# Performance work log

Measured on AMD Instinct MI355X. Metric: run time of the kernel, lower is better.

Reference implementation:

```python
import jax, jax.numpy as jnp
import numpy as np

B_, N, C = 4096, 49, 128
H = 4          # num_heads
NW = 64        # windows per image


def setup_inputs() -> dict:
    key = jax.random.key(0)
    k = jax.random.split(key, 6)
    s = 0.02
    return {
        "x": jax.random.normal(k[0], (B_, N, C), jnp.float32),
        "mask": jax.random.normal(k[1], (NW, N, N), jnp.float32),
        "qkv_w": jax.random.normal(k[2], (3 * C, C), jnp.float32) * s,
        "qkv_b": jax.random.normal(k[3], (3 * C,), jnp.float32) * s,
        "proj_w": jax.random.normal(k[4], (C, C), jnp.float32) * s,
        "proj_b": jax.random.normal(k[5], (C,), jnp.float32) * s,
    }


def reference(x, mask, qkv_w, qkv_b, proj_w, proj_b):
    b, n, c = x.shape
    hd = c // H
    scale = hd ** -0.5
    # fused QKV projection: [b, n, 3, H, hd] -> [3, b, H, n, hd]
    qkv = (x @ qkv_w.T + qkv_b).reshape(b, n, 3, H, hd)
    qkv = jnp.transpose(qkv, (2, 0, 3, 1, 4))
    q, k, v = qkv[0] * scale, qkv[1], qkv[2]
    attn = jnp.einsum("bhnd,bhmd->bhnm", q, k)  # [b, H, n, n]
    nW = mask.shape[0]
    attn = attn.reshape(b // nW, nW, H, n, n) + mask[None, :, None, :, :]
    attn = jax.nn.softmax(attn.reshape(b, H, n, n), axis=-1)
    out = jnp.einsum("bhnm,bhmd->bhnd", attn, v)
    out = jnp.transpose(out, (0, 2, 1, 3)).reshape(b, n, c)
    return out @ proj_w.T + proj_b
```

## Files before the change

kernel.cpp:

```cpp
#include <hip/hip_runtime.h>
#include <hip/hip_bf16.h>

#define C_DIM 128
#define SCALE 0.17677669529663687f

typedef __attribute__((ext_vector_type(8))) short frag8;
typedef __attribute__((ext_vector_type(4))) float f32x4;

#define HEAD_SZ 7424
#define Q_STR 40
#define VT_STR 72
#define P_STR 72
#define XBF_STR 136
#define SMEM_TOT 29696

__device__ __forceinline__ unsigned short f2b(float x) {
    __hip_bfloat16 h = __float2bfloat16(x);
    return __builtin_bit_cast(unsigned short, h);
}
__device__ __forceinline__ unsigned pk2(float a, float b) {
    return ((unsigned)f2b(b) << 16) | (unsigned)f2b(a);
}

__global__ void convert_weights(const float4* __restrict__ qkvw,
                                const float4* __restrict__ projw,
                                ushort4* __restrict__ wbf) {
    int i = blockIdx.x * 256 + threadIdx.x;
    float4 v = (i < 12288) ? qkvw[i] : projw[i - 12288];
    ushort4 p;
    p.x = f2b(v.x); p.y = f2b(v.y); p.z = f2b(v.z); p.w = f2b(v.w);
    wbf[i] = p;
}

__global__ __launch_bounds__(512, 4) void attn_mfma(
    const float* __restrict__ x,
    const float* __restrict__ mask,
    const float* __restrict__ qkv_b,
    const float* __restrict__ proj_b,
    const unsigned short* __restrict__ wq,
    float* __restrict__ out)
{
    __shared__ __align__(16) unsigned short sm[SMEM_TOT];

    const int b = blockIdx.x, tid = threadIdx.x;
    const int wave = tid >> 6;
    const int h    = wave >> 1;
    const int half = wave & 1;
    const int lane = tid & 63;
    const int n16  = lane & 15;
    const int q    = lane >> 4;

    {
        const float4* xg = (const float4*)(x + (size_t)b * 6272);
        for (int i = tid; i < 1568; i += 512) {
            float4 v = xg[i];
            int row = i >> 5, col = (i & 31) << 2;
            uint2 pk; pk.x = pk2(v.x, v.y); pk.y = pk2(v.z, v.w);
            *(uint2*)&sm[row * XBF_STR + col] = pk;
        }
        if (tid < 510) *(ushort4*)&sm[49 * XBF_STR + tid * 4] = (ushort4){0, 0, 0, 0};
    }
    __syncthreads();

    frag8 xf[2][4];
#pragma unroll
    for (int tt = 0; tt < 2; ++tt)
#pragma unroll
        for (int ks = 0; ks < 4; ++ks)
            xf[tt][ks] = *(const frag8*)&sm[((half * 2 + tt) * 16 + n16) * XBF_STR + ks * 32 + q * 8];
    __syncthreads();

    const int Qb = h * HEAD_SZ, Kb = Qb + 2560, Vb = Qb + 5120, Pb = Qb;

#pragma unroll
    for (int mat = 0; mat < 3; ++mat) {
#pragma unroll
        for (int ct = 0; ct < 2; ++ct) {
            const unsigned short* wrow = wq + (size_t)(mat * C_DIM + h * 32 + ct * 16 + n16) * C_DIM;
            frag8 wf[4];
#pragma unroll
            for (int ks = 0; ks < 4; ++ks) wf[ks] = *(const frag8*)(wrow + ks * 32 + q * 8);
            if (mat < 2) {
                float4 b4 = *(const float4*)(qkv_b + mat * C_DIM + h * 32 + ct * 16 + q * 4);
                const float sc = (mat == 0) ? SCALE : 1.f;
                const int base = (mat == 0) ? Qb : Kb;
#pragma unroll
                for (int tt = 0; tt < 2; ++tt) {
                    f32x4 acc = {0.f, 0.f, 0.f, 0.f};
#pragma unroll
                    for (int ks = 0; ks < 4; ++ks)
                        acc = __builtin_amdgcn_mfma_f32_16x16x32_bf16(wf[ks], xf[tt][ks], acc, 0, 0, 0);
                    uint2 pk;
                    pk.x = pk2((acc[0] + b4.x) * sc, (acc[1] + b4.y) * sc);
                    pk.y = pk2((acc[2] + b4.z) * sc, (acc[3] + b4.w) * sc);
                    *(uint2*)&sm[base + ((half * 2 + tt) * 16 + n16) * Q_STR + ct * 16 + q * 4] = pk;
                }
            } else {
                float bias = qkv_b[2 * C_DIM + h * 32 + ct * 16 + n16];
#pragma unroll
                for (int tt = 0; tt < 2; ++tt) {
                    f32x4 acc = {0.f, 0.f, 0.f, 0.f};
#pragma unroll
                    for (int ks = 0; ks < 4; ++ks)
                        acc = __builtin_amdgcn_mfma_f32_16x16x32_bf16(xf[tt][ks], wf[ks], acc, 0, 0, 0);
                    uint2 pk;
                    pk.x = pk2(acc[0] + bias, acc[1] + bias);
                    pk.y = pk2(acc[2] + bias, acc[3] + bias);
                    *(uint2*)&sm[Vb + (ct * 16 + n16) * VT_STR + (half * 2 + tt) * 16 + q * 4] = pk;
                }
            }
        }
    }
    __syncthreads();

    frag8 qf[2], kf[4];
#pragma unroll
    for (int it = 0; it < 2; ++it)
        qf[it] = *(const frag8*)&sm[Qb + ((half * 2 + it) * 16 + n16) * Q_STR + q * 8];
#pragma unroll
    for (int jt = 0; jt < 4; ++jt)
        kf[jt] = *(const frag8*)&sm[Kb + (jt * 16 + n16) * Q_STR + q * 8];
    __syncthreads();

    const float* mrow = mask + (size_t)(b & 63) * 2401;
    int ii[2];
#pragma unroll
    for (int it = 0; it < 2; ++it) ii[it] = min(half * 32 + it * 16 + n16, 48);

    f32x4 s[4][2];
#pragma unroll
    for (int it = 0; it < 2; ++it) {
#pragma unroll
        for (int jt = 0; jt < 3; ++jt) {
            const float* mp = mrow + ii[it] * 49 + jt * 16 + q * 4;
            s[jt][it] = (f32x4){mp[0], mp[1], mp[2], mp[3]};
        }
        float m48 = (q == 0) ? mrow[ii[it] * 49 + 48] : 0.f;
        s[3][it] = (f32x4){m48, 0.f, 0.f, 0.f};
    }
#pragma unroll
    for (int jt = 0; jt < 4; ++jt)
#pragma unroll
        for (int it = 0; it < 2; ++it)
            s[jt][it] = __builtin_amdgcn_mfma_f32_16x16x32_bf16(kf[jt], qf[it], s[jt][it], 0, 0, 0);

#pragma unroll
    for (int it = 0; it < 2; ++it) {
        float mx = -1e30f;
#pragma unroll
        for (int jt = 0; jt < 4; ++jt)
#pragma unroll
            for (int r = 0; r < 4; ++r)
                if (jt * 16 + q * 4 + r < 49) mx = fmaxf(mx, s[jt][it][r]);
        mx = fmaxf(mx, __shfl_xor(mx, 16));
        mx = fmaxf(mx, __shfl_xor(mx, 32));
        float sum = 0.f;
#pragma unroll
        for (int jt = 0; jt < 4; ++jt)
#pragma unroll
            for (int r = 0; r < 4; ++r) {
                float e = (jt * 16 + q * 4 + r < 49) ? __expf(s[jt][it][r] - mx) : 0.f;
                s[jt][it][r] = e;
                sum += e;
            }
        sum += __shfl_xor(sum, 16);
        sum += __shfl_xor(sum, 32);
        float inv = __builtin_amdgcn_rcpf(sum);
#pragma unroll
        for (int jt = 0; jt < 4; ++jt) {
            uint2 pk;
            pk.x = pk2(s[jt][it][0] * inv, s[jt][it][1] * inv);
            pk.y = pk2(s[jt][it][2] * inv, s[jt][it][3] * inv);
            *(uint2*)&sm[Pb + (half * 32 + it * 16 + n16) * P_STR + jt * 16 + q * 4] = pk;
        }
    }

    frag8 vf[2][2];
#pragma unroll
    for (int ct = 0; ct < 2; ++ct)
#pragma unroll
        for (int ks = 0; ks < 2; ++ks)
            vf[ct][ks] = *(const frag8*)&sm[Vb + (ct * 16 + n16) * VT_STR + ks * 32 + q * 8];
    f32x4 o[2][2];
#pragma unroll
    for (int ct = 0; ct < 2; ++ct)
#pragma unroll
        for (int nt = 0; nt < 2; ++nt) o[ct][nt] = (f32x4){0.f, 0.f, 0.f, 0.f};
#pragma unroll
    for (int nt = 0; nt < 2; ++nt)
#pragma unroll
        for (int ks = 0; ks < 2; ++ks) {
            frag8 pf = *(const frag8*)&sm[Pb + ((half * 2 + nt) * 16 + n16) * P_STR + ks * 32 + q * 8];
#pragma unroll
            for (int ct = 0; ct < 2; ++ct)
                o[ct][nt] = __builtin_amdgcn_mfma_f32_16x16x32_bf16(vf[ct][ks], pf, o[ct][nt], 0, 0, 0);
        }
    __syncthreads();

#pragma unroll
    for (int ct = 0; ct < 2; ++ct)
#pragma unroll
        for (int nt = 0; nt < 2; ++nt) {
            uint2 pk;
            pk.x = pk2(o[ct][nt][0], o[ct][nt][1]);
            pk.y = pk2(o[ct][nt][2], o[ct][nt][3]);
            *(uint2*)&sm[((half * 2 + nt) * 16 + n16) * XBF_STR + h * 32 + ct * 16 + q * 4] = pk;
        }
    __syncthreads();

    const unsigned short* pw = wq + 49152;
    frag8 wf2[4];
#pragma unroll
    for (int ks = 0; ks < 4; ++ks)
        wf2[ks] = *(const frag8*)(pw + (size_t)(wave * 16 + n16) * C_DIM + ks * 32 + q * 8);
    float4 b4 = *(const float4*)(proj_b + wave * 16 + q * 4);
    float* outb = out + (size_t)b * 6272;
#pragma unroll
    for (int nt = 0; nt < 4; ++nt) {
        f32x4 acc = {0.f, 0.f, 0.f, 0.f};
#pragma unroll
        for (int ks = 0; ks < 4; ++ks) {
            frag8 af = *(const frag8*)&sm[(nt * 16 + n16) * XBF_STR + ks * 32 + q * 8];
            acc = __builtin_amdgcn_mfma_f32_16x16x32_bf16(wf2[ks], af, acc, 0, 0, 0);
        }
        int tok = nt * 16 + n16;
        if (tok < 49)
            *(float4*)&outb[tok * C_DIM + wave * 16 + q * 4] =
                make_float4(acc[0] + b4.x, acc[1] + b4.y, acc[2] + b4.z, acc[3] + b4.w);
    }
}

extern "C" void kernel_launch(void* const* d_in, const int* in_sizes, int n_in,
                              void* d_out, int out_size, void* d_ws, size_t ws_size,
                              hipStream_t stream) {
    const float* x      = (const float*)d_in[0];
    const float* mask   = (const float*)d_in[1];
    const float* qkv_b  = (const float*)d_in[3];
    const float* proj_b = (const float*)d_in[5];

    unsigned short* wbf = (unsigned short*)d_ws;
    convert_weights<<<64, 256, 0, stream>>>((const float4*)d_in[2],
                                            (const float4*)d_in[4],
                                            (ushort4*)wbf);
    attn_mfma<<<4096, 512, 0, stream>>>(x, mask, qkv_b, proj_b, wbf, (float*)d_out);
}
```

Baseline: 293.1 us.

## Use one wave per head with 256-thread blocks and fewer barriers

Changes the block from 8 waves (two per head, each handling half the tokens) to 4 waves, one per head, so each wave computes all 49 tokens for its head. This removes several block-wide barriers, because Q/K/V/P stay private to each wave, and the per-head buffers now live beyond the activation buffer so x no longer has to be rewritten. The projection weights and biases are loaded at kernel start to hide global latency, and each wave computes two output column tiles. In exchange, each wave holds more registers (xf[4][4], s[4][4], wf2) and there are fewer waves per block, which may reduce latency hiding and occupancy.

```diff
diff --git a/kernel.cpp b/kernel.cpp
--- a/kernel.cpp
+++ b/kernel.cpp
@@ -7,12 +7,15 @@
 typedef __attribute__((ext_vector_type(8))) short frag8;
 typedef __attribute__((ext_vector_type(4))) float f32x4;
 
-#define HEAD_SZ 7424
+#define XACT_STR 136
+#define HEAD_OFF 6800
+#define HEAD_SZ  6304
+#define KOFF 2000
+#define VOFF 4000
 #define Q_STR 40
 #define VT_STR 72
 #define P_STR 72
-#define XBF_STR 136
-#define SMEM_TOT 29696
+#define SMEM_TOT 32016
 
 __device__ __forceinline__ unsigned short f2b(float x) {
     __hip_bfloat16 h = __float2bfloat16(x);
@@ -32,7 +35,7 @@
     wbf[i] = p;
 }
 
-__global__ __launch_bounds__(512, 4) void attn_mfma(
+__global__ __launch_bounds__(256, 2) void attn_mfma(
     const float* __restrict__ x,
     const float* __restrict__ mask,
     const float* __restrict__ qkv_b,
@@ -43,34 +46,43 @@
     __shared__ __align__(16) unsigned short sm[SMEM_TOT];
 
     const int b = blockIdx.x, tid = threadIdx.x;
-    const int wave = tid >> 6;
-    const int h    = wave >> 1;
-    const int half = wave & 1;
+    const int h    = tid >> 6;
     const int lane = tid & 63;
     const int n16  = lane & 15;
     const int q    = lane >> 4;
 
+    const unsigned short* pw = wq + 49152;
+    frag8 wf2[2][4];
+#pragma unroll
+    for (int ct = 0; ct < 2; ++ct)
+#pragma unroll
+        for (int ks = 0; ks < 4; ++ks)
+            wf2[ct][ks] = *(const frag8*)(pw + (size_t)(h * 32 + ct * 16 + n16) * C_DIM + ks * 32 + q * 8);
+    float4 pb4[2];
+#pragma unroll
+    for (int ct = 0; ct < 2; ++ct)
+        pb4[ct] = *(const float4*)(proj_b + h * 32 + ct * 16 + q * 4);
+
     {
         const float4* xg = (const float4*)(x + (size_t)b * 6272);
-        for (int i = tid; i < 1568; i += 512) {
+        for (int i = tid; i < 1568; i += 256) {
             float4 v = xg[i];
             int row = i >> 5, col = (i & 31) << 2;
             uint2 pk; pk.x = pk2(v.x, v.y); pk.y = pk2(v.z, v.w);
-            *(uint2*)&sm[row * XBF_STR + col] = pk;
-        }
-        if (tid < 510) *(ushort4*)&sm[49 * XBF_STR + tid * 4] = (ushort4){0, 0, 0, 0};
+            *(uint2*)&sm[row * XACT_STR + col] = pk;
+        }
     }
     __syncthreads();
 
-    frag8 xf[2][4];
-#pragma unroll
-    for (int tt = 0; tt < 2; ++tt)
+    frag8 xf[4][4];
+#pragma unroll
+    for (int tt = 0; tt < 4; ++tt)
 #pragma unroll
         for (int ks = 0; ks < 4; ++ks)
-            xf[tt][ks] = *(const frag8*)&sm[((half * 2 + tt) * 16 + n16) * XBF_STR + ks * 32 + q * 8];
+            xf[tt][ks] = *(const frag8*)&sm[min(tt * 16 + n16, 48) * XACT_STR + ks * 32 + q * 8];
     __syncthreads();
 
-    const int Qb = h * HEAD_SZ, Kb = Qb + 2560, Vb = Qb + 5120, Pb = Qb;
+    const int Hb = HEAD_OFF + h * HEAD_SZ;
 
 #pragma unroll
     for (int mat = 0; mat < 3; ++mat) {
@@ -83,9 +95,9 @@
             if (mat < 2) {
                 float4 b4 = *(const float4*)(qkv_b + mat * C_DIM + h * 32 + ct * 16 + q * 4);
                 const float sc = (mat == 0) ? SCALE : 1.f;
-                const int base = (mat == 0) ? Qb : Kb;
-#pragma unroll
-                for (int tt = 0; tt < 2; ++tt) {
+                const int base = Hb + ((mat == 0) ? 0 : KOFF);
+#pragma unroll
+                for (int tt = 0; tt < 4; ++tt) {
                     f32x4 acc = {0.f, 0.f, 0.f, 0.f};
 #pragma unroll
                     for (int ks = 0; ks < 4; ++ks)
@@ -93,12 +105,12 @@
                     uint2 pk;
                     pk.x = pk2((acc[0] + b4.x) * sc, (acc[1] + b4.y) * sc);
                     pk.y = pk2((acc[2] + b4.z) * sc, (acc[3] + b4.w) * sc);
-                    *(uint2*)&sm[base + ((half * 2 + tt) * 16 + n16) * Q_STR + ct * 16 + q * 4] = pk;
+                    *(uint2*)&sm[base + min(tt * 16 + n16, 49) * Q_STR + ct * 16 + q * 4] = pk;
                 }
             } else {
                 float bias = qkv_b[2 * C_DIM + h * 32 + ct * 16 + n16];
 #pragma unroll
-                for (int tt = 0; tt < 2; ++tt) {
+                for (int tt = 0; tt < 4; ++tt) {
                     f32x4 acc = {0.f, 0.f, 0.f, 0.f};
 #pragma unroll
                     for (int ks = 0; ks < 4; ++ks)
@@ -106,46 +118,39 @@
                     uint2 pk;
                     pk.x = pk2(acc[0] + bias, acc[1] + bias);
                     pk.y = pk2(acc[2] + bias, acc[3] + bias);
-                    *(uint2*)&sm[Vb + (ct * 16 + n16) * VT_STR + (half * 2 + tt) * 16 + q * 4] = pk;
+                    *(uint2*)&sm[Hb + VOFF + (ct * 16 + n16) * VT_STR + tt * 16 + q * 4] = pk;
                 }
             }
         }
     }
-    __syncthreads();
-
-    frag8 qf[2], kf[4];
-#pragma unroll
-    for (int it = 0; it < 2; ++it)
-        qf[it] = *(const frag8*)&sm[Qb + ((half * 2 + it) * 16 + n16) * Q_STR + q * 8];
+
+    frag8 qf[4], kf[4];
+#pragma unroll
+    for (int t = 0; t < 4; ++t) {
+        qf[t] = *(const frag8*)&sm[Hb + (t * 16 + n16) * Q_STR + q * 8];
+        kf[t] = *(const frag8*)&sm[Hb + KOFF + (t * 16 + n16) * Q_STR + q * 8];
+    }
+    const float* mrow = mask + (size_t)(b & 63) * 2401;
+    f32x4 s[4][4];
+#pragma unroll
+    for (int it = 0; it < 4; ++it) {
+        int ii = min(it * 16 + n16, 48);
+#pragma unroll
+        for (int jt = 0; jt < 3; ++jt) {
+            const float* mp = mrow + ii * 49 + jt * 16 + q * 4;
+            s[jt][it] = (f32x4){mp[0], mp[1], mp[2], mp[3]};
+        }
+        float m48 = (q == 0) ? mrow[ii * 49 + 48] : 0.f;
+        s[3][it] = (f32x4){m48, 0.f, 0.f, 0.f};
+    }
 #pragma unroll
     for (int jt = 0; jt < 4; ++jt)
-        kf[jt] = *(const frag8*)&sm[Kb + (jt * 16 + n16) * Q_STR + q * 8];
-    __syncthreads();
-
-    const float* mrow = mask + (size_t)(b & 63) * 2401;
-    int ii[2];
-#pragma unroll
-    for (int it = 0; it < 2; ++it) ii[it] = min(half * 32 + it * 16 + n16, 48);
-
-    f32x4 s[4][2];
-#pragma unroll
-    for (int it = 0; it < 2; ++it) {
-#pragma unroll
-        for (int jt = 0; jt < 3; ++jt) {
-            const float* mp = mrow + ii[it] * 49 + jt * 16 + q * 4;
-            s[jt][it] = (f32x4){mp[0], mp[1], mp[2], mp[3]};
-        }
-        float m48 = (q == 0) ? mrow[ii[it] * 49 + 48] : 0.f;
-        s[3][it] = (f32x4){m48, 0.f, 0.f, 0.f};
-    }
-#pragma unroll
-    for (int jt = 0; jt < 4; ++jt)
-#pragma unroll
-        for (int it = 0; it < 2; ++it)
+#pragma unroll
+        for (int it = 0; it < 4; ++it)
             s[jt][it] = __builtin_amdgcn_mfma_f32_16x16x32_bf16(kf[jt], qf[it], s[jt][it], 0, 0, 0);
 
 #pragma unroll
-    for (int it = 0; it < 2; ++it) {
+    for (int it = 0; it < 4; ++it) {
         float mx = -1e30f;
 #pragma unroll
         for (int jt = 0; jt < 4; ++jt)
@@ -171,7 +176,7 @@
             uint2 pk;
             pk.x = pk2(s[jt][it][0] * inv, s[jt][it][1] * inv);
             pk.y = pk2(s[jt][it][2] * inv, s[jt][it][3] * inv);
-            *(uint2*)&sm[Pb + (half * 32 + it * 16 + n16) * P_STR + jt * 16 + q * 4] = pk;
+            *(uint2*)&sm[Hb + min(it * 16 + n16, 49) * P_STR + jt * 16 + q * 4] = pk;
         }
     }
 
@@ -180,53 +185,52 @@
     for (int ct = 0; ct < 2; ++ct)
 #pragma unroll
         for (int ks = 0; ks < 2; ++ks)
-            vf[ct][ks] = *(const frag8*)&sm[Vb + (ct * 16 + n16) * VT_STR + ks * 32 + q * 8];
-    f32x4 o[2][2];
-#pragma unroll
-    for (int ct = 0; ct < 2; ++ct)
-#pragma unroll
-        for (int nt = 0; nt < 2; ++nt) o[ct][nt] = (f32x4){0.f, 0.f, 0.f, 0.f};
-#pragma unroll
-    for (int nt = 0; nt < 2; ++nt)
+            vf[ct][ks] = *(const frag8*)&sm[Hb + VOFF + (ct * 16 + n16) * VT_STR + ks * 32 + q * 8];
+    f32x4 o[2][4];
+#pragma unroll
+    for (int ct = 0; ct < 2; ++ct)
+#pragma unroll
+        for (int nt = 0; nt < 4; ++nt) o[ct][nt] = (f32x4){0.f, 0.f, 0.f, 0.f};
+#pragma unroll
+    for (int nt = 0; nt < 4; ++nt)
 #pragma unroll
         for (int ks = 0; ks < 2; ++ks) {
-            frag8 pf = *(const frag8*)&sm[Pb + ((half * 2 + nt) * 16 + n16) * P_STR + ks * 32 + q * 8];
+            frag8 pf = *(const frag8*)&sm[Hb + min(nt * 16 + n16, 49) * P_STR + ks * 32 + q * 8];
 #pragma unroll
             for (int ct = 0; ct < 2; ++ct)
                 o[ct][nt] = __builtin_amdgcn_mfma_f32_16x16x32_bf16(vf[ct][ks], pf, o[ct][nt], 0, 0, 0);
         }
-    __syncthreads();
-
-#pragma unroll
-    for (int ct = 0; ct < 2; ++ct)
-#pragma unroll
-        for (int nt = 0; nt < 2; ++nt) {
+
+#pragma unroll
+    for (int ct = 0; ct < 2; ++ct)
+#pragma unroll
+        for (int nt = 0; nt < 4; ++nt) {
             uint2 pk;
             pk.x = pk2(o[ct][nt][0], o[ct][nt][1]);
             pk.y = pk2(o[ct][nt][2], o[ct][nt][3]);
-            *(uint2*)&sm[((half * 2 + nt) * 16 + n16) * XBF_STR + h * 32 + ct * 16 + q * 4] = pk;
+            *(uint2*)&sm[min(nt * 16 + n16, 49) * XACT_STR + h * 32 + ct * 16 + q * 4] = pk;
         }
     __syncthreads();
 
-    const unsigned short* pw = wq + 49152;
-    frag8 wf2[4];
-#pragma unroll
-    for (int ks = 0; ks < 4; ++ks)
-        wf2[ks] = *(const frag8*)(pw + (size_t)(wave * 16 + n16) * C_DIM + ks * 32 + q * 8);
-    float4 b4 = *(const float4*)(proj_b + wave * 16 + q * 4);
     float* outb = out + (size_t)b * 6272;
 #pragma unroll
     for (int nt = 0; nt < 4; ++nt) {
-        f32x4 acc = {0.f, 0.f, 0.f, 0.f};
-#pragma unroll
-        for (int ks = 0; ks < 4; ++ks) {
-            frag8 af = *(const frag8*)&sm[(nt * 16 + n16) * XBF_STR + ks * 32 + q * 8];
-            acc = __builtin_amdgcn_mfma_f32_16x16x32_bf16(wf2[ks], af, acc, 0, 0, 0);
-        }
+        frag8 af[4];
+#pragma unroll
+        for (int ks = 0; ks < 4; ++ks)
+            af[ks] = *(const frag8*)&sm[min(nt * 16 + n16, 48) * XACT_STR + ks * 32 + q * 8];
         int tok = nt * 16 + n16;
-        if (tok < 49)
-            *(float4*)&outb[tok * C_DIM + wave * 16 + q * 4] =
-                make_float4(acc[0] + b4.x, acc[1] + b4.y, acc[2] + b4.z, acc[3] + b4.w);
+#pragma unroll
+        for (int ct = 0; ct < 2; ++ct) {
+            f32x4 acc = {0.f, 0.f, 0.f, 0.f};
+#pragma unroll
+            for (int ks = 0; ks < 4; ++ks)
+                acc = __builtin_amdgcn_mfma_f32_16x16x32_bf16(wf2[ct][ks], af[ks], acc, 0, 0, 0);
+            if (tok < 49)
+                *(float4*)&outb[tok * C_DIM + h * 32 + ct * 16 + q * 4] =
+                    make_float4(acc[0] + pb4[ct].x, acc[1] + pb4[ct].y,
+                                acc[2] + pb4[ct].z, acc[3] + pb4[ct].w);
+        }
     }
 }
 
@@ -242,5 +246,5 @@
     convert_weights<<<64, 256, 0, stream>>>((const float4*)d_in[2],
                                             (const float4*)d_in[4],
                                             (ushort4*)wbf);
-    attn_mfma<<<4096, 512, 0, stream>>>(x, mask, qkv_b, proj_b, wbf, (float*)d_out);
-}
+    attn_mfma<<<4096, 256, 0, stream>>>(x, mask, qkv_b, proj_b, wbf, (float*)d_out);
+}
```

After: 273.3 us. -6.7%, faster.
